# Kernel optimization log

Hardware: AMD Instinct MI355X
Metric: run time of the kernel (lower is better)

The kernel has to match this reference:

```python
import jax, jax.numpy as jnp
import numpy as np
from math import log2, ceil

HEADS, DIM_HEAD, BLOCK, EPS = 16, 64, 16, 1e-8


def setup_inputs() -> dict:
    key = jax.random.key(0)
    k1, k2, k3, k4 = jax.random.split(key, 4)
    b, n, dim = 4, 4096, 1024
    inner = HEADS * DIM_HEAD
    return {
        "x": jax.random.normal(k1, (b, n, dim), jnp.float32),
        "w_qkv": jax.random.normal(k2, (inner * 3, dim), jnp.float32) * 0.02,
        "w_out": jax.random.normal(k3, (dim, inner), jnp.float32) * 0.02,
        "b_out": jax.random.normal(k4, (dim,), jnp.float32) * 0.02,
    }


def reference(x, w_qkv, w_out, b_out):
    b, n, dim = x.shape
    pad_to_len = 2 ** ceil(log2(n))
    if pad_to_len != n:
        x = jnp.pad(x, ((0, 0), (0, pad_to_len - n), (0, 0)))
    qkv = x @ w_qkv.T  # torch Linear (no bias): weight is [out, in]
    q, k, v = jnp.split(qkv, 3, axis=-1)

    def split_heads(t):
        return t.reshape(b, pad_to_len, HEADS, DIM_HEAD).transpose(0, 2, 1, 3).reshape(b * HEADS, pad_to_len, DIM_HEAD)

    q = split_heads(q) * DIM_HEAD ** -0.5
    k = split_heads(k)
    v = split_heads(v)

    num_levels = int(log2(pad_to_len // BLOCK)) - 1
    # hierarchical coarsening: q,k averaged over pairs, v summed over pairs
    qkvs = [(q, k, v)]
    for _ in range(num_levels):
        q = q.reshape(q.shape[0], -1, 2, DIM_HEAD).mean(2)
        k = k.reshape(k.shape[0], -1, 2, DIM_HEAD).mean(2)
        v = v.reshape(v.shape[0], -1, 2, DIM_HEAD).sum(2)
        qkvs.append((q, k, v))

    neg_max = -jnp.finfo(x.dtype).max
    idx = jnp.arange(pad_to_len)
    Ysum = jnp.zeros((b * HEADS, pad_to_len, DIM_HEAD), x.dtype)
    Asum = jnp.zeros((b * HEADS, pad_to_len), x.dtype)

    for lvl, (ql, kl, vl) in enumerate(qkvs):
        B = ql.shape[0]
        nb = ql.shape[1] // BLOCK  # number of blocks at this level
        ql = ql.reshape(B, nb, BLOCK, DIM_HEAD)
        kl = kl.reshape(B, nb, BLOCK, DIM_HEAD)
        vl = vl.reshape(B, nb, BLOCK, DIM_HEAD)
        if lvl == 0:
            # finest level: causal diagonal block attention
            S = jnp.einsum('bnid,bnjd->bnij', ql, kl)
            S = jnp.where(jnp.triu(jnp.ones((BLOCK, BLOCK), bool), 1), neg_max, S)
            S = S - S.max(-1, keepdims=True)
            A = jnp.exp(S)
            y = jnp.einsum('bnij,bnjd->bnid', A, vl).reshape(B, pad_to_len, DIM_HEAD)
            Av = A.sum(-1).reshape(B, pad_to_len)
        else:
            # off-diagonal: second block of each pair attends to first block of pair
            q2 = ql.reshape(B, nb // 2, 2, BLOCK, DIM_HEAD)[:, :, 1]
            k1b = kl.reshape(B, nb // 2, 2, BLOCK, DIM_HEAD)[:, :, 0]  # flip_every_two then take [:,1]
            v1b = vl.reshape(B, nb // 2, 2, BLOCK, DIM_HEAD)[:, :, 0]
            S = jnp.einsum('bnid,bnjd->bnij', q2, k1b)
            S = S - S.max(-1, keepdims=True)
            A = jnp.exp(S)
            y = jnp.einsum('bnij,bnjd->bnid', A, v1b)  # [B, nb/2, BLOCK, d]
            Av = A.sum(-1)
            # zero-pad first block of each pair, flatten blocks back to sequence
            y = jnp.pad(y[:, :, None], ((0, 0), (0, 0), (1, 0), (0, 0), (0, 0))).reshape(B, -1, DIM_HEAD)
            Av = jnp.pad(Av[:, :, None], ((0, 0), (0, 0), (1, 0), (0, 0))).reshape(B, -1)
            # expand coarsened positions to full resolution (consecutive repeats)
            y = jnp.repeat(y, 2 ** lvl, axis=1)
            Av = jnp.repeat(Av, 2 ** lvl, axis=1)
        # causal keep-mask: max original index inside the coarsened key group <= query index
        seq_key = (idx >> lvl << lvl) + (2 ** lvl - 1)
        keep = seq_key <= idx  # at lvl=0 seq_key == idx -> keep all
        Ysum = Ysum + jnp.where(keep[None, :, None], y, 0.0)
        Asum = Asum + jnp.where(keep[None, :], Av, 0.0)

    out = Ysum / (Asum + EPS)[..., None]
    out = out.reshape(b, HEADS, pad_to_len, DIM_HEAD).transpose(0, 2, 1, 3).reshape(b, pad_to_len, HEADS * DIM_HEAD)
    out = out @ w_out.T + b_out
    return out[:, :n]
```

## Files before the change

kernel.cpp:

```cpp
#include <hip/hip_runtime.h>

typedef __bf16 bf16_t;
typedef __attribute__((ext_vector_type(8))) __bf16 bf16x8;
typedef __attribute__((ext_vector_type(4))) float f32x4;

#define MFMA(a,b,c) __builtin_amdgcn_mfma_f32_16x16x32_bf16(a,b,c,0,0,0)

static __device__ __forceinline__ unsigned short f2bfbits(float f){
  unsigned int u = __builtin_bit_cast(unsigned int, f);
  return (unsigned short)((u + 0x7FFFu + ((u >> 16) & 1u)) >> 16);
}
static __device__ __forceinline__ float bits2f(unsigned int b){
  return __builtin_bit_cast(float, b << 16);
}
static __device__ __forceinline__ void gl_lds16(const void* g, void* l){
  __builtin_amdgcn_global_load_lds(
      (const __attribute__((address_space(1))) void*)(g),
      (__attribute__((address_space(3))) void*)(l), 16, 0, 0);
}
static __device__ __forceinline__ void unpack8(uint4 raw, float* f){
  f[0]=bits2f(raw.x&0xFFFFu); f[1]=bits2f(raw.x>>16);
  f[2]=bits2f(raw.y&0xFFFFu); f[3]=bits2f(raw.y>>16);
  f[4]=bits2f(raw.z&0xFFFFu); f[5]=bits2f(raw.z>>16);
  f[6]=bits2f(raw.w&0xFFFFu); f[7]=bits2f(raw.w>>16);
}

__global__ __launch_bounds__(256) void cvt_all(const float* __restrict__ x,
                                               const float* __restrict__ wqkv,
                                               const float* __restrict__ wout,
                                               unsigned short* __restrict__ xb,
                                               unsigned short* __restrict__ wqb,
                                               unsigned short* __restrict__ wob){
  const long n4 = 5242880;
  const long stride = (long)gridDim.x * 256;
  for (long i = (long)blockIdx.x * 256 + threadIdx.x; i < n4; i += stride){
    const float* in; unsigned short* out; long e;
    if (i < 4194304){ in = x; out = xb; e = i; }
    else if (i < 4980736){ in = wqkv; out = wqb; e = i - 4194304; }
    else { in = wout; out = wob; e = i - 4980736; }
    float4 v = *(const float4*)(in + e * 4);
    unsigned long long pack = (unsigned long long)f2bfbits(v.x)
      | ((unsigned long long)f2bfbits(v.y) << 16)
      | ((unsigned long long)f2bfbits(v.z) << 32)
      | ((unsigned long long)f2bfbits(v.w) << 48);
    *(unsigned long long*)(out + e * 4) = pack;
  }
}

template<int MODE>
__global__ __launch_bounds__(512, 2) void gemm256(
    const unsigned short* __restrict__ A, const unsigned short* __restrict__ B,
    const int K, const int nbx,
    unsigned short* __restrict__ oq, unsigned short* __restrict__ ok2, unsigned short* __restrict__ ov,
    float* __restrict__ outp, const float* __restrict__ bias)
{
  __shared__ char lds[131072];
  const int t = threadIdx.x;
  const int lane = t & 63, wid = t >> 6;
  const int wr = wid >> 2, wc = wid & 3;
  const int r16 = lane & 15, g = lane >> 4;

  const int nb = gridDim.x, cpx = nb >> 3;
  const int lin = (blockIdx.x & 7) * cpx + (blockIdx.x >> 3);
  const int by = lin / nbx, bx = lin - by * nbx;
  const long row0 = (long)by * 256, col0 = (long)bx * 256;

  const unsigned short* gA[2]; const unsigned short* gB[2];
  int ldsoff[2];
  #pragma unroll
  for (int r2 = 0; r2 < 2; ++r2){
    const int flat = r2*512 + t;
    const int row = flat >> 2;
    const int sg = (flat & 3) ^ ((row >> 1) & 3);
    gA[r2] = A + (row0 + row) * K + sg*8;
    gB[r2] = B + (col0 + row) * K + sg*8;
    ldsoff[r2] = (r2*512 + wid*64) * 16;
  }

  f32x4 acc[8][4];
  #pragma unroll
  for (int m = 0; m < 8; ++m)
    #pragma unroll
    for (int n = 0; n < 4; ++n)
      acc[m][n] = (f32x4){0.f, 0.f, 0.f, 0.f};

  const int nk = K >> 5;

  #define STAGE_H(s, half) do{                                  \
    const long koff = (long)(s) * 32;                           \
    char* sb = lds + ((s) & 3) * 32768;                         \
    gl_lds16(gA[half] + koff, sb + ldsoff[half]);               \
    gl_lds16(gB[half] + koff, sb + 16384 + ldsoff[half]);       \
  }while(0)

  STAGE_H(0,0); STAGE_H(0,1);
  STAGE_H(1,0); STAGE_H(1,1);
  STAGE_H(2,0); STAGE_H(2,1);
  asm volatile("s_waitcnt vmcnt(8)" ::: "memory");
  __builtin_amdgcn_s_barrier();

  for (int i = 0; i < nk; ++i){
    const char* sl = lds + (i & 3) * 32768;
    bf16x8 bfr[4], afr[8];
    #pragma unroll
    for (int n = 0; n < 4; ++n){
      const int br = wc*64 + n*16 + r16;
      bfr[n] = *(const bf16x8*)(sl + 16384 + br*64 + ((g ^ ((br >> 1) & 3)) << 4));
    }
    #pragma unroll
    for (int m = 0; m < 4; ++m){
      const int ar = wr*128 + m*16 + r16;
      afr[m] = *(const bf16x8*)(sl + ar*64 + ((g ^ ((ar >> 1) & 3)) << 4));
    }
    if (i + 3 < nk) STAGE_H(i + 3, 0);
    __builtin_amdgcn_s_barrier();
    asm volatile("s_waitcnt lgkmcnt(0)" ::: "memory");
    __builtin_amdgcn_sched_barrier(0);
    __builtin_amdgcn_s_setprio(1);
    #pragma unroll
    for (int m = 0; m < 4; ++m)
      #pragma unroll
      for (int n = 0; n < 4; ++n)
        acc[m][n] = MFMA(afr[m], bfr[n], acc[m][n]);
    __builtin_amdgcn_s_setprio(0);
    __builtin_amdgcn_s_barrier();

    #pragma unroll
    for (int m = 4; m < 8; ++m){
      const int ar = wr*128 + m*16 + r16;
      afr[m] = *(const bf16x8*)(sl + ar*64 + ((g ^ ((ar >> 1) & 3)) << 4));
    }
    if (i + 3 < nk){
      STAGE_H(i + 3, 1);
      asm volatile("s_waitcnt vmcnt(8)" ::: "memory");
    } else if (i == nk - 3){
      asm volatile("s_waitcnt vmcnt(4)" ::: "memory");
    } else if (i == nk - 2){
      asm volatile("s_waitcnt vmcnt(0)" ::: "memory");
    }
    __builtin_amdgcn_s_barrier();
    asm volatile("s_waitcnt lgkmcnt(0)" ::: "memory");
    __builtin_amdgcn_sched_barrier(0);
    __builtin_amdgcn_s_setprio(1);
    #pragma unroll
    for (int m = 4; m < 8; ++m)
      #pragma unroll
      for (int n = 0; n < 4; ++n)
        acc[m][n] = MFMA(afr[m], bfr[n], acc[m][n]);
    __builtin_amdgcn_s_setprio(0);
    __builtin_amdgcn_s_barrier();
  }
  #undef STAGE_H

  if (MODE == 0){
    __syncthreads();
    const int which = (int)(col0 >> 10);
    const int h = (int)((col0 & 1023) >> 6) + wc;
    const float sc = (which == 0) ? 0.125f : 1.0f;
    unsigned short* st = (unsigned short*)lds + wid*8192;
    #pragma unroll
    for (int pass = 0; pass < 2; ++pass){
      #pragma unroll
      for (int mm = 0; mm < 4; ++mm)
        #pragma unroll
        for (int n = 0; n < 4; ++n)
          #pragma unroll
          for (int q2 = 0; q2 < 4; ++q2)
            st[(mm*16 + g*4 + q2)*72 + n*16 + r16] = f2bfbits(acc[pass*4 + mm][n][q2] * sc);
      const long prow0 = row0 + wr*128 + pass*64;
      if (which < 2){
        unsigned short* dst = (which == 0) ? oq : ok2;
        #pragma unroll
        for (int rd = 0; rd < 8; ++rd){
          const int rl = rd*8 + (lane >> 3);
          const int gr = lane & 7;
          uint4 v = *(const uint4*)&st[rl*72 + gr*8];
          const long ii = prow0 + rl;
          const int b_ = (int)(ii >> 12), pos = (int)(ii & 4095);
          *(uint4*)&dst[(((long)b_*16 + h)*4096 + pos)*64 + gr*8] = v;
        }
      } else {
        #pragma unroll
        for (int rd = 0; rd < 8; ++rd){
          const int blk = rd >> 1;
          const int d = (rd & 1)*32 + (lane >> 1);
          const int kkh = lane & 1;
          unsigned short tmp[8];
          #pragma unroll
          for (int j = 0; j < 8; ++j)
            tmp[j] = st[(blk*16 + kkh*8 + j)*72 + d];
          uint4 v;
          v.x = (unsigned int)tmp[0] | ((unsigned int)tmp[1] << 16);
          v.y = (unsigned int)tmp[2] | ((unsigned int)tmp[3] << 16);
          v.z = (unsigned int)tmp[4] | ((unsigned int)tmp[5] << 16);
          v.w = (unsigned int)tmp[6] | ((unsigned int)tmp[7] << 16);
          const long posblk = (prow0 >> 4) + blk;
          const int b_ = (int)(posblk >> 8), blkg = (int)(posblk & 255);
          *(uint4*)&ov[(((long)b_*16 + h)*256 + blkg)*1024 + d*16 + kkh*8] = v;
        }
      }
      __builtin_amdgcn_sched_barrier(0);
    }
  } else {
    #pragma unroll
    for (int n = 0; n < 4; ++n){
      const long j = col0 + wc*64 + n*16 + r16;
      const float bi = bias[j];
      #pragma unroll
      for (int m = 0; m < 8; ++m){
        const long ib = row0 + wr*128 + m*16 + g*4;
        #pragma unroll
        for (int q2 = 0; q2 < 4; ++q2)
          outp[(ib + q2)*1024 + j] = acc[m][n][q2] + bi;
      }
    }
  }
}

__global__ __launch_bounds__(256) void coarsen(
    const unsigned short* __restrict__ q0, const unsigned short* __restrict__ k0,
    const unsigned short* __restrict__ vt0,
    unsigned short* __restrict__ qch, unsigned short* __restrict__ kch,
    unsigned short* __restrict__ vch)
{
  __shared__ float Abuf[128*65];
  __shared__ float Bbuf[64*65];
  const int t = threadIdx.x;
  const int chunk = blockIdx.x;
  const int bh = blockIdx.y;
  const int arr = blockIdx.z;
  if (arr < 2){
    const unsigned short* src = (arr == 0) ? q0 : k0;
    const long sbase = ((long)bh*4096 + (long)chunk*128) * 64;
    #pragma unroll
    for (int it = 0; it < 4; ++it){
      const int idx = it*2048 + t*8;
      uint4 raw = *(const uint4*)(src + sbase + idx);
      float f[8]; unpack8(raw, f);
      const int rowb = idx >> 6, colb = idx & 63;
      #pragma unroll
      for (int j = 0; j < 8; ++j) Abuf[rowb*65 + colb + j] = f[j];
    }
  } else {
    const long sbase = ((long)bh*256 + (long)chunk*8) * 1024;
    #pragma unroll
    for (int it = 0; it < 4; ++it){
      const int flat = it*2048 + t*8;
      const int blk = flat >> 10, rem = flat & 1023;
      const int d = rem >> 4, kk0 = rem & 15;
      uint4 raw = *(const uint4*)(vt0 + sbase + flat);
      float f[8]; unpack8(raw, f);
      #pragma unroll
      for (int j = 0; j < 8; ++j) Abuf[(blk*16 + kk0 + j)*65 + d] = f[j];
    }
  }
  __syncthreads();
  float* cur = Abuf; float* nxt = Bbuf;
  int rows = 128;
  const int Spre[8] = {0, 0, 1024, 1536, 1792, 1920, 1984, 2016};
  for (int l = 1; l <= 7; ++l){
    rows >>= 1;
    const int P = 2048 >> l;
    const long base = (long)Spre[l] * 4096;
    for (int e = t; e < rows*64; e += 256){
      const int p = e >> 6, d = e & 63;
      const float a = cur[(2*p)*65 + d], b2 = cur[(2*p + 1)*65 + d];
      const float val = (arr == 2) ? (a + b2) : 0.5f*(a + b2);
      nxt[p*65 + d] = val;
      const int pl = chunk*rows + p;
      const int cb = pl >> 4, ci = cb >> 1;
      if (arr == 0){
        if (cb & 1) qch[base + ((long)bh*P + ci*16 + (pl & 15))*64 + d] = f2bfbits(val);
      } else if (arr == 1){
        if (!(cb & 1)) kch[base + ((long)bh*P + ci*16 + (pl & 15))*64 + d] = f2bfbits(val);
      } else if (rows < 16){
        if (!(cb & 1)) vch[base + (long)bh*P*64 + ci*1024 + d*16 + (pl & 15)] = f2bfbits(val);
      }
    }
    __syncthreads();
    if (arr == 2 && rows >= 16){
      const int nblk = rows >> 4;
      for (int oe = t; oe < nblk*1024; oe += 256){
        const int bl = oe >> 10, rem = oe & 1023;
        const int cb = chunk*nblk + bl;
        if (cb & 1) continue;
        const int d = rem >> 4, kk = rem & 15;
        vch[base + (long)bh*P*64 + (long)(cb>>1)*1024 + rem] = f2bfbits(nxt[(bl*16 + kk)*65 + d]);
      }
    }
    float* tmp = cur; cur = nxt; nxt = tmp;
  }
}

__global__ __launch_bounds__(256) void attn_fused(
    const unsigned short* __restrict__ q0, const unsigned short* __restrict__ k0,
    const unsigned short* __restrict__ vt0,
    const unsigned short* __restrict__ qch, const unsigned short* __restrict__ kch,
    const unsigned short* __restrict__ vch,
    unsigned short* __restrict__ ybf)
{
  const int lane = threadIdx.x & 63;
  const int w = threadIdx.x >> 6;
  const int B0 = blockIdx.x * 4 + w;
  const int bh = blockIdx.y;
  const int b_ = bh >> 4, h = bh & 15;
  const int r = lane & 15, g = lane >> 4;
  __shared__ float accs_all[4][16*64];
  __shared__ float denoms_all[4][16];
  float* accs = accs_all[w];
  float* denoms = denoms_all[w];

  {
    const long base = ((long)bh*4096 + (long)B0*16) * 64;
    const bf16x8 ka0 = *(const bf16x8*)(k0 + base + r*64 + g*8);
    const bf16x8 ka1 = *(const bf16x8*)(k0 + base + r*64 + g*8 + 32);
    const bf16x8 qb0 = *(const bf16x8*)(q0 + base + r*64 + g*8);
    const bf16x8 qb1 = *(const bf16x8*)(q0 + base + r*64 + g*8 + 32);
    f32x4 s = {0.f,0.f,0.f,0.f};
    s = MFMA(ka0, qb0, s);
    s = MFMA(ka1, qb1, s);

    float p[4];
    float mx = -3.402823466e38f;
    #pragma unroll
    for (int j = 0; j < 4; ++j){
      const int c = g*4 + j;
      p[j] = (c <= r) ? s[j] : -3.402823466e38f;
      mx = fmaxf(mx, p[j]);
    }
    mx = fmaxf(mx, __shfl_xor(mx, 16));
    mx = fmaxf(mx, __shfl_xor(mx, 32));
    float rs = 0.f;
    #pragma unroll
    for (int j = 0; j < 4; ++j){
      const int c = g*4 + j;
      p[j] = (c <= r) ? __expf(p[j] - mx) : 0.f;
      rs += p[j];
    }
    rs += __shfl_xor(rs, 16);
    rs += __shfl_xor(rs, 32);

    float x16[4], x32[4], x48[4];
    #pragma unroll
    for (int j = 0; j < 4; ++j){
      x16[j] = __shfl_xor(p[j], 16);
      x32[j] = __shfl_xor(p[j], 32);
      x48[j] = __shfl_xor(p[j], 48);
    }
    bf16x8 af;
    #pragma unroll
    for (int j = 0; j < 4; ++j){
      const float lo = (g == 0) ? p[j]   : (g == 1) ? x48[j] : 0.f;
      const float hi = (g == 0) ? x16[j] : (g == 1) ? x32[j] : 0.f;
      af[j]   = (bf16_t)lo;
      af[j+4] = (bf16_t)hi;
    }
    const unsigned short* vt = vt0 + ((long)bh*256 + B0) * 1024;
    #pragma unroll
    for (int nb = 0; nb < 4; ++nb){
      bf16x8 bv;
      #pragma unroll
      for (int j = 0; j < 8; ++j) bv[j] = (bf16_t)0.f;
      if (g < 2) bv = *(const bf16x8*)(vt + (nb*16 + r)*16 + g*8);
      f32x4 y = {0.f,0.f,0.f,0.f};
      y = MFMA(af, bv, y);
      #pragma unroll
      for (int q2 = 0; q2 < 4; ++q2)
        accs[(g*4 + q2)*64 + nb*16 + r] = y[q2];
    }
    if (g == 0) denoms[r] = rs;
  }

  const int Spre[8] = {0, 0, 1024, 1536, 1792, 1920, 1984, 2016};
  for (int l = 1; l <= 7; ++l){
    int nr, lo, cb;
    if (l <= 4){
      nr = 16 >> l;
      lo = (B0 & ((1 << l) - 1)) << (4 - l);
      cb = B0 >> l;
    } else {
      const int m = 1 << (l - 4);
      if ((B0 & (m - 1)) != m - 1) continue;
      const int qrow = ((B0 + 1) >> (l - 4)) - 1;
      cb = qrow >> 4; lo = qrow & 15; nr = 1;
    }
    if (!(cb & 1)) continue;
    const int ci = cb >> 1;
    const int P = 2048 >> l;
    const long base = (long)Spre[l] * 4096;
    const long qb_base = base + ((long)bh*P + ci*16) * 64;
    const long kv_base = base + (long)bh*P*64 + (long)ci*1024;

    const bf16x8 ka0 = *(const bf16x8*)(kch + qb_base + r*64 + g*8);
    const bf16x8 ka1 = *(const bf16x8*)(kch + qb_base + r*64 + g*8 + 32);
    const bf16x8 qb0 = *(const bf16x8*)(qch + qb_base + r*64 + g*8);
    const bf16x8 qb1 = *(const bf16x8*)(qch + qb_base + r*64 + g*8 + 32);
    f32x4 s = {0.f,0.f,0.f,0.f};
    s = MFMA(ka0, qb0, s);
    s = MFMA(ka1, qb1, s);

    float p[4];
    float mx = fmaxf(fmaxf(s[0], s[1]), fmaxf(s[2], s[3]));
    mx = fmaxf(mx, __shfl_xor(mx, 16));
    mx = fmaxf(mx, __shfl_xor(mx, 32));
    float rs = 0.f;
    #pragma unroll
    for (int j = 0; j < 4; ++j){ p[j] = __expf(s[j] - mx); rs += p[j]; }
    rs += __shfl_xor(rs, 16);
    rs += __shfl_xor(rs, 32);

    float x16[4], x32[4], x48[4];
    #pragma unroll
    for (int j = 0; j < 4; ++j){
      x16[j] = __shfl_xor(p[j], 16);
      x32[j] = __shfl_xor(p[j], 32);
      x48[j] = __shfl_xor(p[j], 48);
    }
    bf16x8 af;
    #pragma unroll
    for (int j = 0; j < 4; ++j){
      const float lo2 = (g == 0) ? p[j]   : (g == 1) ? x48[j] : 0.f;
      const float hi2 = (g == 0) ? x16[j] : (g == 1) ? x32[j] : 0.f;
      af[j]   = (bf16_t)lo2;
      af[j+4] = (bf16_t)hi2;
    }
    #pragma unroll
    for (int nb = 0; nb < 4; ++nb){
      bf16x8 bv;
      #pragma unroll
      for (int j = 0; j < 8; ++j) bv[j] = (bf16_t)0.f;
      if (g < 2) bv = *(const bf16x8*)(vch + kv_base + (nb*16 + r)*16 + g*8);
      f32x4 y = {0.f,0.f,0.f,0.f};
      y = MFMA(af, bv, y);
      #pragma unroll
      for (int q2 = 0; q2 < 4; ++q2){
        const int row = g*4 + q2;
        if (row >= lo && row < lo + nr){
          const int ii = (((cb*16 + row + 1) << l) - 1) - (B0 << 4);
          accs[ii*64 + nb*16 + r] += y[q2];
        }
      }
    }
    if (g == 0 && r >= lo && r < lo + nr){
      const int ii = (((cb*16 + r + 1) << l) - 1) - (B0 << 4);
      denoms[ii] += rs;
    }
  }

  const int row = lane >> 2, d0 = (lane & 3) * 16;
  const float inv = 1.f / (denoms[row] + 1e-8f);
  unsigned int wv[8];
  #pragma unroll
  for (int j2 = 0; j2 < 8; ++j2){
    const float a = accs[row*64 + d0 + 2*j2]      * inv;
    const float b2 = accs[row*64 + d0 + 2*j2 + 1] * inv;
    wv[j2] = (unsigned int)f2bfbits(a) | ((unsigned int)f2bfbits(b2) << 16);
  }
  uint4* dst = (uint4*)(ybf + ((long)b_*4096 + B0*16 + row)*1024 + h*64 + d0);
  dst[0] = make_uint4(wv[0], wv[1], wv[2], wv[3]);
  dst[1] = make_uint4(wv[4], wv[5], wv[6], wv[7]);
}

extern "C" void kernel_launch(void* const* d_in, const int* in_sizes, int n_in,
                              void* d_out, int out_size, void* d_ws, size_t ws_size,
                              hipStream_t stream){
  const float* x    = (const float*)d_in[0];
  const float* wqkv = (const float*)d_in[1];
  const float* wout = (const float*)d_in[2];
  const float* bout = (const float*)d_in[3];
  float* out = (float*)d_out;
  char* ws = (char*)d_ws;

  unsigned short* wqb = (unsigned short*)(ws + 0L);
  unsigned short* wob = (unsigned short*)(ws + 6291456L);
  unsigned short* xb  = (unsigned short*)(ws + 8388608L);
  unsigned short* q0  = (unsigned short*)(ws + 41943040L);
  unsigned short* k0  = (unsigned short*)(ws + 75497472L);
  unsigned short* vt0 = (unsigned short*)(ws + 109051904L);
  unsigned short* qch = (unsigned short*)(ws + 142606336L);
  unsigned short* kch = (unsigned short*)(ws + 159252480L);
  unsigned short* vch = (unsigned short*)(ws + 175898624L);
  unsigned short* ybf = xb;

  cvt_all<<<2048, 256, 0, stream>>>(x, wqkv, wout, xb, wqb, wob);

  gemm256<0><<<768, 512, 0, stream>>>(xb, wqb, 1024, 12, q0, k0, vt0, nullptr, nullptr);
  coarsen<<<dim3(32,64,3), 256, 0, stream>>>(q0, k0, vt0, qch, kch, vch);
  attn_fused<<<dim3(64,64), 256, 0, stream>>>(q0, k0, vt0, qch, kch, vch, ybf);
  gemm256<1><<<256, 512, 0, stream>>>(ybf, wob, 1024, 4, nullptr, nullptr, nullptr, out, bout);
}
```

Measured before the change: 308.3 us.

## Restructure GEMM mainloop: direct-register B loads, BK=64 double buffering, LDS-staged output

```diff
diff --git a/kernel.cpp b/kernel.cpp
--- a/kernel.cpp
+++ b/kernel.cpp
@@ -65,17 +65,19 @@
   const int by = lin / nbx, bx = lin - by * nbx;
   const long row0 = (long)by * 256, col0 = (long)bx * 256;
 
-  const unsigned short* gA[2]; const unsigned short* gB[2];
-  int ldsoff[2];
+  const unsigned short* gA[4]; int ldsoff[4];
   #pragma unroll
-  for (int r2 = 0; r2 < 2; ++r2){
+  for (int r2 = 0; r2 < 4; ++r2){
     const int flat = r2*512 + t;
-    const int row = flat >> 2;
-    const int sg = (flat & 3) ^ ((row >> 1) & 3);
-    gA[r2] = A + (row0 + row) * K + sg*8;
-    gB[r2] = B + (col0 + row) * K + sg*8;
+    const int row = flat >> 3, slot = flat & 7;
+    const int slotg = slot ^ (row & 7);
+    gA[r2] = A + (row0 + row) * K + slotg*8;
     ldsoff[r2] = (r2*512 + wid*64) * 16;
   }
+  const unsigned short* pB[4];
+  #pragma unroll
+  for (int n = 0; n < 4; ++n)
+    pB[n] = B + (col0 + wc*64 + n*16 + r16) * (long)K + g*8;
 
   f32x4 acc[8][4];
   #pragma unroll
@@ -84,73 +86,65 @@
     for (int n = 0; n < 4; ++n)
       acc[m][n] = (f32x4){0.f, 0.f, 0.f, 0.f};
 
-  const int nk = K >> 5;
-
-  #define STAGE_H(s, half) do{                                  \
-    const long koff = (long)(s) * 32;                           \
-    char* sb = lds + ((s) & 3) * 32768;                         \
-    gl_lds16(gA[half] + koff, sb + ldsoff[half]);               \
-    gl_lds16(gB[half] + koff, sb + 16384 + ldsoff[half]);       \
+  const int nk = K >> 6;
+
+  #define SA(tt) do{                                              \
+    char* sb = lds + ((tt)&1)*32768;                              \
+    gl_lds16(gA[0] + (tt)*64, sb + ldsoff[0]);                    \
+    gl_lds16(gA[1] + (tt)*64, sb + ldsoff[1]);                    \
+    gl_lds16(gA[2] + (tt)*64, sb + ldsoff[2]);                    \
+    gl_lds16(gA[3] + (tt)*64, sb + ldsoff[3]);                    \
   }while(0)
-
-  STAGE_H(0,0); STAGE_H(0,1);
-  STAGE_H(1,0); STAGE_H(1,1);
-  STAGE_H(2,0); STAGE_H(2,1);
-  asm volatile("s_waitcnt vmcnt(8)" ::: "memory");
+  #define LB(tt, dst) do{                                         \
+    _Pragma("unroll")                                             \
+    for (int n = 0; n < 4; ++n){                                  \
+      dst[n*2]   = *(const bf16x8*)(pB[n] + (tt)*64);             \
+      dst[n*2+1] = *(const bf16x8*)(pB[n] + (tt)*64 + 32);        \
+    }                                                             \
+  }while(0)
+  #define GTILE(tv, CUR, NXT) do{                                 \
+    const int tt = (tv);                                          \
+    const char* sl = lds + (tt&1)*32768;                          \
+    const bool more = (tt + 1 < nk);                              \
+    if (more){ SA(tt+1); LB(tt+1, NXT); }                         \
+    _Pragma("unroll")                                             \
+    for (int mp = 0; mp < 4; ++mp){                               \
+      bf16x8 afr[2][2];                                           \
+      _Pragma("unroll")                                           \
+      for (int mi = 0; mi < 2; ++mi)                              \
+        _Pragma("unroll")                                         \
+        for (int kk = 0; kk < 2; ++kk){                           \
+          const int row = wr*128 + (mp*2 + mi)*16 + r16;          \
+          afr[mi][kk] = *(const bf16x8*)(sl + row*128 + (((kk*4 + g) ^ (row & 7)) << 4)); \
+        }                                                         \
+      asm volatile("s_waitcnt lgkmcnt(0)" ::: "memory");          \
+      __builtin_amdgcn_sched_barrier(0);                          \
+      __builtin_amdgcn_s_setprio(1);                              \
+      _Pragma("unroll")                                           \
+      for (int mi = 0; mi < 2; ++mi)                              \
+        _Pragma("unroll")                                         \
+        for (int n = 0; n < 4; ++n)                               \
+          _Pragma("unroll")                                       \
+          for (int kk = 0; kk < 2; ++kk)                          \
+            acc[mp*2 + mi][n] = MFMA(afr[mi][kk], CUR[n*2+kk], acc[mp*2 + mi][n]); \
+      __builtin_amdgcn_s_setprio(0);                              \
+    }                                                             \
+    if (more) asm volatile("s_waitcnt vmcnt(0)" ::: "memory");    \
+    __builtin_amdgcn_s_barrier();                                 \
+  }while(0)
+
+  bf16x8 bAr[8], bBr[8];
+  SA(0); LB(0, bAr);
+  asm volatile("s_waitcnt vmcnt(0)" ::: "memory");
   __builtin_amdgcn_s_barrier();
 
-  for (int i = 0; i < nk; ++i){
-    const char* sl = lds + (i & 3) * 32768;
-    bf16x8 bfr[4], afr[8];
-    #pragma unroll
-    for (int n = 0; n < 4; ++n){
-      const int br = wc*64 + n*16 + r16;
-      bfr[n] = *(const bf16x8*)(sl + 16384 + br*64 + ((g ^ ((br >> 1) & 3)) << 4));
-    }
-    #pragma unroll
-    for (int m = 0; m < 4; ++m){
-      const int ar = wr*128 + m*16 + r16;
-      afr[m] = *(const bf16x8*)(sl + ar*64 + ((g ^ ((ar >> 1) & 3)) << 4));
-    }
-    if (i + 3 < nk) STAGE_H(i + 3, 0);
-    __builtin_amdgcn_s_barrier();
-    asm volatile("s_waitcnt lgkmcnt(0)" ::: "memory");
-    __builtin_amdgcn_sched_barrier(0);
-    __builtin_amdgcn_s_setprio(1);
-    #pragma unroll
-    for (int m = 0; m < 4; ++m)
-      #pragma unroll
-      for (int n = 0; n < 4; ++n)
-        acc[m][n] = MFMA(afr[m], bfr[n], acc[m][n]);
-    __builtin_amdgcn_s_setprio(0);
-    __builtin_amdgcn_s_barrier();
-
-    #pragma unroll
-    for (int m = 4; m < 8; ++m){
-      const int ar = wr*128 + m*16 + r16;
-      afr[m] = *(const bf16x8*)(sl + ar*64 + ((g ^ ((ar >> 1) & 3)) << 4));
-    }
-    if (i + 3 < nk){
-      STAGE_H(i + 3, 1);
-      asm volatile("s_waitcnt vmcnt(8)" ::: "memory");
-    } else if (i == nk - 3){
-      asm volatile("s_waitcnt vmcnt(4)" ::: "memory");
-    } else if (i == nk - 2){
-      asm volatile("s_waitcnt vmcnt(0)" ::: "memory");
-    }
-    __builtin_amdgcn_s_barrier();
-    asm volatile("s_waitcnt lgkmcnt(0)" ::: "memory");
-    __builtin_amdgcn_sched_barrier(0);
-    __builtin_amdgcn_s_setprio(1);
-    #pragma unroll
-    for (int m = 4; m < 8; ++m)
-      #pragma unroll
-      for (int n = 0; n < 4; ++n)
-        acc[m][n] = MFMA(afr[m], bfr[n], acc[m][n]);
-    __builtin_amdgcn_s_setprio(0);
-    __builtin_amdgcn_s_barrier();
-  }
-  #undef STAGE_H
+  for (int kt = 0; kt < nk; kt += 2){
+    GTILE(kt,     bAr, bBr);
+    GTILE(kt + 1, bBr, bAr);
+  }
+  #undef SA
+  #undef LB
+  #undef GTILE
 
   if (MODE == 0){
     __syncthreads();
@@ -202,17 +196,26 @@
       __builtin_amdgcn_sched_barrier(0);
     }
   } else {
-    #pragma unroll
-    for (int n = 0; n < 4; ++n){
-      const long j = col0 + wc*64 + n*16 + r16;
-      const float bi = bias[j];
-      #pragma unroll
-      for (int m = 0; m < 8; ++m){
-        const long ib = row0 + wr*128 + m*16 + g*4;
+    __syncthreads();
+    float* stf = (float*)(lds + wid*4352);
+    float bi[4];
+    #pragma unroll
+    for (int n = 0; n < 4; ++n) bi[n] = bias[col0 + wc*64 + n*16 + r16];
+    #pragma unroll
+    for (int mm = 0; mm < 8; ++mm){
+      #pragma unroll
+      for (int n = 0; n < 4; ++n)
         #pragma unroll
         for (int q2 = 0; q2 < 4; ++q2)
-          outp[(ib + q2)*1024 + j] = acc[m][n][q2] + bi;
+          stf[(g*4 + q2)*68 + n*16 + r16] = acc[mm][n][q2] + bi[n];
+      const long prow0 = row0 + wr*128 + mm*16;
+      #pragma unroll
+      for (int rr = 0; rr < 4; ++rr){
+        const int rowl = (lane >> 4) + rr*4;
+        f32x4 v = *(const f32x4*)&stf[rowl*68 + (lane & 15)*4];
+        *(f32x4*)&outp[(prow0 + rowl)*1024 + col0 + wc*64 + (lane & 15)*4] = v;
       }
+      __builtin_amdgcn_sched_barrier(0);
     }
   }
 }
```

Result: slower. 362.7 us (+17.7%).
